# Kernel optimization log

Hardware: AMD Instinct MI355X
Metric: run time of the kernel (lower is better)

## Reference

```python
import jax, jax.numpy as jnp
import numpy as np

REF_MIC = 0
LOAD = 0.001 / np.sqrt(2.0)  # diagonal loading added to both real and imag parts


def _to_complex(x):
    # x: (N, 2, ...) real/imag stacked -> complex (N, ...)
    return x[:, 0] + 1j * x[:, 1]


def setup_inputs() -> dict:
    key = jax.random.key(0)
    k1, k2, k3 = jax.random.split(key, 3)
    N, C, T, F = 8, 16, 300, 257
    mixture = jax.random.normal(k1, (N, 2, C, T, F), dtype=jnp.float32)
    target = jax.random.normal(k2, (N, 2, C, T, F), dtype=jnp.float32)
    steering_vector = jax.random.normal(k3, (N, 2, C, F), dtype=jnp.float32)
    return {"mixture": mixture, "target": target, "steering_vector": steering_vector}


def reference(mixture, target, steering_vector):
    N, _, C, T, F = mixture.shape
    y = _to_complex(mixture)  # (N, C, T, F)
    x = _to_complex(target)   # (N, C, T, F)

    # Spatial covariance of mixture, mean over time frames (sum/T), fused einsum
    # phi[n,f] = (1/T) * sum_t y[n,:,t,f] y[n,:,t,f]^H  -> (N, F, C, C)
    phi = jnp.einsum('nctf,ndtf->nfcd', y, jnp.conj(y)) / T
    eye = jnp.eye(C, dtype=phi.dtype)
    # original adds load to BOTH real and imag diagonals (broadcast over RI dim)
    phi = phi + (LOAD + 1j * LOAD) * eye
    phi_inv = jnp.linalg.inv(phi)  # (N, F, C, C)

    # Cross covariance between mixture and reference-mic target
    A = jnp.transpose(y, (0, 3, 2, 1))            # (N, F, T, C)
    b = jnp.transpose(x[:, REF_MIC], (0, 2, 1))   # (N, F, T)
    mu_a = jnp.mean(A, axis=(0, 2), keepdims=True)  # mean over batch and time
    mu_b = jnp.mean(b, axis=(0, 2), keepdims=True)
    # mean over T of (A-mu_a)(b-mu_b)^H -> (N, F, C)
    phi_yx0 = jnp.mean((A - mu_a) * jnp.conj(b - mu_b)[..., None], axis=2)

    # MWF weights: w = phi_inv @ phi_yx0  -> (N, F, C)
    w = jnp.einsum('nfcd,nfd->nfc', phi_inv, phi_yx0)

    # Beamform: X_bf[n,t,f] = w[n,f]^H y[n,:,t,f]
    Xbf = jnp.einsum('nfc,nctf->ntf', jnp.conj(w), y)  # (N, T, F)

    # Back to real/imag stacked (N, 2, 1, T, F) matching torch output layout
    out = jnp.stack([Xbf.real, Xbf.imag], axis=1)[:, :, None]
    return out
```

## Files before the change

### kernel.cpp

```cpp
#include <hip/hip_runtime.h>

#define N_     8
#define C_     16
#define T_     300
#define F_     257
#define CC_    256
#define TF_    (T_*F_)
#define CTF_   (C_*TF_)
#define N2CTF_ (2*CTF_)

#define FT_    32
#define NFT_   9
#define TS_    5
#define RST_   35
#define SROWS_ 88
#define SCNT_  (SROWS_*RST_)

#define LOADC  7.0710678118654755e-04f

__device__ __forceinline__ float2 cmul(float2 a, float2 b) {
  return make_float2(a.x*b.x - a.y*b.y, a.x*b.y + a.y*b.x);
}
__device__ __forceinline__ float2 cmulc(float2 a, float2 b) {
  return make_float2(a.x*b.x + a.y*b.y, a.y*b.x - a.x*b.y);
}
__device__ __forceinline__ float2 cdiv(float2 a, float2 b) {
  float inv = 1.0f / (b.x*b.x + b.y*b.y);
  return make_float2((a.x*b.x + a.y*b.y)*inv, (a.y*b.x - a.x*b.y)*inv);
}
__device__ __forceinline__ float2 cadd(float2 a, float2 b){ return make_float2(a.x+b.x, a.y+b.y); }
__device__ __forceinline__ float2 csub(float2 a, float2 b){ return make_float2(a.x-b.x, a.y-b.y); }

template<int TCH>
__global__ __launch_bounds__(512, 1) void k1_cov(const float* __restrict__ mix,
                                                 const float* __restrict__ tgt,
                                                 float2* __restrict__ phi_p,
                                                 float2* __restrict__ syx_p,
                                                 float2* __restrict__ sy_p,
                                                 float2* __restrict__ sx_p) {
  __shared__ float2 ys[2][SCNT_];
  const int tid = threadIdx.x;
  const int ft = blockIdx.x, tc = blockIdx.y, n = blockIdx.z;
  const int fbase = ft * FT_;
  const int t0 = tc * TCH;
  const int fl = tid & 31;
  const int g  = tid >> 5;
  const int c0 = (g & 3) * 4;
  const int d0 = (g >> 2) * 4;
  const bool sThread = (g < 4);
  const bool xLoader = (tid < 256);

  const float* mixN = mix + n * N2CTF_;
  const float* tgtN = tgt + n * N2CTF_;

  const int srow = tid >> 5;
  const int f_ld = min(fbase + fl, F_ - 1);
  const float* ybase = mixN + srow * TF_ + f_ld;
  const int xts = min(srow, TS_ - 1);
  const float* xbase = tgtN + f_ld;

  float2 acc[4][4];
  #pragma unroll
  for (int i = 0; i < 4; ++i)
    #pragma unroll
    for (int j = 0; j < 4; ++j) acc[i][j] = make_float2(0.f, 0.f);
  float2 syx[4], sy[4], sx = make_float2(0.f, 0.f);
  #pragma unroll
  for (int i = 0; i < 4; ++i) { syx[i] = make_float2(0.f,0.f); sy[i] = make_float2(0.f,0.f); }

  float lr[6], li[6];
  {
    #pragma unroll
    for (int k = 0; k < TS_; ++k) {
      const float* p = ybase + (t0 + k) * F_;
      lr[k] = p[0]; li[k] = p[CTF_];
    }
    if (xLoader) { const float* p = xbase + (t0 + xts) * F_; lr[5] = p[0]; li[5] = p[CTF_]; }
    #pragma unroll
    for (int k = 0; k < TS_; ++k)
      ys[0][(k * 16 + srow) * RST_ + fl] = make_float2(lr[k], li[k]);
    if (xLoader) ys[0][(80 + srow) * RST_ + fl] = make_float2(lr[5], li[5]);
  }

  constexpr int NS = TCH / TS_;
  for (int stg = 0; stg < NS; ++stg) {
    __syncthreads();
    const bool more = (stg + 1 < NS);
    if (more) {
      const int tS = t0 + (stg + 1) * TS_;
      #pragma unroll
      for (int k = 0; k < TS_; ++k) {
        const float* p = ybase + (tS + k) * F_;
        lr[k] = p[0]; li[k] = p[CTF_];
      }
      if (xLoader) { const float* p = xbase + (tS + xts) * F_; lr[5] = p[0]; li[5] = p[CTF_]; }
    }
    const float2* buf = ys[stg & 1];
    #pragma unroll
    for (int tl = 0; tl < TS_; ++tl) {
      const int rb = tl * 16;
      float2 a[4], b[4];
      #pragma unroll
      for (int i = 0; i < 4; ++i) a[i] = buf[(rb + c0 + i) * RST_ + fl];
      #pragma unroll
      for (int j = 0; j < 4; ++j) b[j] = buf[(rb + d0 + j) * RST_ + fl];
      #pragma unroll
      for (int i = 0; i < 4; ++i)
        #pragma unroll
        for (int j = 0; j < 4; ++j) {
          acc[i][j].x += a[i].x * b[j].x + a[i].y * b[j].y;
          acc[i][j].y += a[i].y * b[j].x - a[i].x * b[j].y;
        }
      if (sThread) {
        float2 xv = buf[(80 + tl) * RST_ + fl];
        #pragma unroll
        for (int i = 0; i < 4; ++i) {
          syx[i].x += a[i].x * xv.x + a[i].y * xv.y;
          syx[i].y += a[i].y * xv.x - a[i].x * xv.y;
          sy[i].x += a[i].x; sy[i].y += a[i].y;
        }
        if (g == 0) { sx.x += xv.x; sx.y += xv.y; }
      }
    }
    if (more) {
      float2* nb = ys[(stg + 1) & 1];
      #pragma unroll
      for (int k = 0; k < TS_; ++k)
        nb[(k * 16 + srow) * RST_ + fl] = make_float2(lr[k], li[k]);
      if (xLoader) nb[(80 + srow) * RST_ + fl] = make_float2(lr[5], li[5]);
    }
  }

  const int f = fbase + fl;
  if (f < F_) {
    const int tcn = tc * N_ + n;
    float2* pb = phi_p + ((size_t)tcn * F_ + f) * CC_;
    #pragma unroll
    for (int i = 0; i < 4; ++i) {
      float2* p = pb + (c0 + i) * 16 + d0;
      #pragma unroll
      for (int j = 0; j < 4; ++j) p[j] = acc[i][j];
    }
    if (sThread) {
      float2* s1 = syx_p + ((size_t)tcn * F_ + f) * C_ + c0;
      float2* s2 = sy_p  + ((size_t)tcn * F_ + f) * C_ + c0;
      #pragma unroll
      for (int i = 0; i < 4; ++i) { s1[i] = syx[i]; s2[i] = sy[i]; }
      if (g == 0) sx_p[(size_t)tcn * F_ + f] = sx;
    }
  }
}

template<int TCP>
__global__ __launch_bounds__(256) void k2_solve(const float2* __restrict__ phi_p,
                                                const float2* __restrict__ syx_p,
                                                const float2* __restrict__ sy_p,
                                                const float2* __restrict__ sx_p,
                                                float* __restrict__ wre,
                                                float* __restrict__ wim) {
  __shared__ float2 M[16 * 17];
  __shared__ float2 fac[16];
  __shared__ float2 ld_sy[TCP * N_ * C_];
  __shared__ float2 ld_syx[TCP * C_];
  __shared__ float2 ld_sx[TCP * N_];
  __shared__ float2 muB_s, sxO_s;
  const int f = blockIdx.x, n = blockIdx.y;
  const int tid = threadIdx.x;
  const int i = tid >> 4, j = tid & 15;

  float2 s = make_float2(0.f, 0.f);
  for (int tc = 0; tc < TCP; ++tc) {
    float2 v = phi_p[((size_t)(tc * N_ + n) * F_ + f) * CC_ + tid];
    s.x += v.x; s.y += v.y;
  }
  if (i == j) { s.x += (float)T_ * LOADC; s.y += (float)T_ * LOADC; }
  M[i * 17 + j] = s;

  for (int idx = tid; idx < TCP * N_ * C_; idx += 256) {
    int tcn = idx >> 4, c = idx & 15;
    ld_sy[idx] = sy_p[((size_t)tcn * F_ + f) * C_ + c];
  }
  for (int idx = tid; idx < TCP * C_; idx += 256) {
    int tc = idx >> 4, c = idx & 15;
    ld_syx[idx] = syx_p[((size_t)(tc * N_ + n) * F_ + f) * C_ + c];
  }
  for (int idx = tid; idx < TCP * N_; idx += 256) {
    ld_sx[idx] = sx_p[(size_t)idx * F_ + f];
  }
  __syncthreads();

  float2 muA_r = make_float2(0.f,0.f), ownY = make_float2(0.f,0.f), ownYX = make_float2(0.f,0.f);
  if (tid < 16) {
    float2 allY = make_float2(0.f,0.f);
    for (int tcn = 0; tcn < TCP * N_; ++tcn) allY = cadd(allY, ld_sy[tcn * C_ + tid]);
    for (int tc = 0; tc < TCP; ++tc) {
      ownY  = cadd(ownY,  ld_sy[(tc * N_ + n) * C_ + tid]);
      ownYX = cadd(ownYX, ld_syx[tc * C_ + tid]);
    }
    const float invNT = 1.0f / ((float)N_ * (float)T_);
    muA_r = make_float2(allY.x * invNT, allY.y * invNT);
  }
  if (tid == 16) {
    float2 own = make_float2(0.f,0.f), all = make_float2(0.f,0.f);
    for (int tc = 0; tc < TCP; ++tc)
      for (int nn = 0; nn < N_; ++nn) {
        float2 v = ld_sx[tc * N_ + nn];
        all = cadd(all, v);
        if (nn == n) own = cadd(own, v);
      }
    const float invNT = 1.0f / ((float)N_ * (float)T_);
    muB_s = make_float2(all.x * invNT, all.y * invNT);
    sxO_s = own;
  }
  __syncthreads();

  if (tid < 16) {
    float2 r = ownYX;
    r = csub(r, cmulc(muA_r, sxO_s));
    r = csub(r, cmulc(ownY, muB_s));
    float2 t3 = cmulc(muA_r, muB_s);
    r.x += (float)T_ * t3.x; r.y += (float)T_ * t3.y;
    M[tid * 17 + 16] = r;
  }
  __syncthreads();

  for (int k = 0; k < 16; ++k) {
    if (tid < 16) {
      fac[tid] = (tid == k) ? make_float2(0.f,0.f)
                            : cdiv(M[tid * 17 + k], M[k * 17 + k]);
    }
    __syncthreads();
    if (i != k) {
      float2 fi = fac[i];
      M[i * 17 + j] = csub(M[i * 17 + j], cmul(fi, M[k * 17 + j]));
      if (j == 15) M[i * 17 + 16] = csub(M[i * 17 + 16], cmul(fi, M[k * 17 + 16]));
    }
    __syncthreads();
  }
  if (tid < 16) {
    float2 w = cdiv(M[tid * 17 + 16], M[tid * 17 + tid]);
    wre[(n * C_ + tid) * F_ + f] = w.x;
    wim[(n * C_ + tid) * F_ + f] = w.y;
  }
}

#define TB3_ 3
__global__ __launch_bounds__(256) void k3_bf(const float* __restrict__ mix,
                                             const float* __restrict__ wre,
                                             const float* __restrict__ wim,
                                             float* __restrict__ out) {
  const int tg = blockIdx.x, n = blockIdx.y;
  const int t0 = tg * TB3_;
  const float* mixN = mix + n * N2CTF_;
  const float* wR = wre + n * C_ * F_;
  const float* wI = wim + n * C_ * F_;
  float* outN = out + n * 2 * TF_;
  for (int f = threadIdx.x; f < F_; f += 256) {
    float wr[16], wi[16];
    #pragma unroll
    for (int c = 0; c < 16; ++c) { wr[c] = wR[c * F_ + f]; wi[c] = wI[c * F_ + f]; }
    #pragma unroll
    for (int tt = 0; tt < TB3_; ++tt) {
      int t = t0 + tt;
      const float* yb = mixN + t * F_ + f;
      float xr = 0.f, xi = 0.f;
      #pragma unroll
      for (int c = 0; c < 16; ++c) {
        float yr = yb[c * TF_];
        float yi = yb[CTF_ + c * TF_];
        xr += wr[c] * yr + wi[c] * yi;
        xi += wr[c] * yi - wi[c] * yr;
      }
      outN[t * F_ + f] = xr;
      outN[TF_ + t * F_ + f] = xi;
    }
  }
}

template<int TCP>
static void launch_all(const float* mix, const float* tgt, float* ws, float* out,
                       hipStream_t stream) {
  constexpr int TCH = T_ / TCP;
  static_assert(TCH * TCP == T_ && TCH % TS_ == 0, "chunking");
  float2* phi_p = (float2*)ws;
  float2* syx_p = phi_p + (size_t)TCP * N_ * F_ * CC_;
  float2* sy_p  = syx_p + (size_t)TCP * N_ * F_ * C_;
  float2* sx_p  = sy_p  + (size_t)TCP * N_ * F_ * C_;
  float*  wre   = (float*)(sx_p + (size_t)TCP * N_ * F_);
  float*  wim   = wre + N_ * C_ * F_;
  k1_cov<TCH><<<dim3(NFT_, TCP, N_), dim3(512), 0, stream>>>(mix, tgt, phi_p, syx_p, sy_p, sx_p);
  k2_solve<TCP><<<dim3(F_, N_), dim3(256), 0, stream>>>(phi_p, syx_p, sy_p, sx_p, wre, wim);
  k3_bf<<<dim3(T_ / TB3_, N_), dim3(256), 0, stream>>>(mix, wre, wim, out);
}

static size_t ws_need_bytes(int tcp) {
  size_t fl = (size_t)tcp * N_ * F_ * (2*CC_ + 2*C_ + 2*C_ + 2) + 2ull * N_ * C_ * F_;
  return fl * 4;
}

extern "C" void kernel_launch(void* const* d_in, const int* in_sizes, int n_in,
                              void* d_out, int out_size, void* d_ws, size_t ws_size,
                              hipStream_t stream) {
  const float* mix = (const float*)d_in[0];
  const float* tgt = (const float*)d_in[1];
  float* out = (float*)d_out;
  float* ws  = (float*)d_ws;
  if (ws_size >= ws_need_bytes(12))      launch_all<12>(mix, tgt, ws, out, stream);
  else if (ws_size >= ws_need_bytes(6))  launch_all<6>(mix, tgt, ws, out, stream);
  else if (ws_size >= ws_need_bytes(2))  launch_all<2>(mix, tgt, ws, out, stream);
  else                                   launch_all<1>(mix, tgt, ws, out, stream);
}
```

Measured before the change: 267.3 us.

## Split solve into reduction and single-wave elimination kernels, simplify beamform

Splits the per-frequency solve into two kernels. The first reduces the partial covariances and cross terms into an augmented matrix stored in global memory. The second runs Gauss-Jordan elimination with a single 64-thread wave, each thread updating four columns, instead of 256 threads with a separate factor array. This is meant to cut idle threads and per-step barrier cost during elimination, at the price of an extra launch and a global round trip for the matrix. The beamform kernel now processes one time frame per block instead of three, giving more blocks but reloading the weights per frame.

```diff
diff --git a/kernel.cpp b/kernel.cpp
--- a/kernel.cpp
+++ b/kernel.cpp
@@ -15,6 +15,8 @@
 #define RST_   35
 #define SROWS_ 88
 #define SCNT_  (SROWS_*RST_)
+
+#define MREC_  272
 
 #define LOADC  7.0710678118654755e-04f
 
@@ -152,14 +154,11 @@
 }
 
 template<int TCP>
-__global__ __launch_bounds__(256) void k2_solve(const float2* __restrict__ phi_p,
-                                                const float2* __restrict__ syx_p,
-                                                const float2* __restrict__ sy_p,
-                                                const float2* __restrict__ sx_p,
-                                                float* __restrict__ wre,
-                                                float* __restrict__ wim) {
-  __shared__ float2 M[16 * 17];
-  __shared__ float2 fac[16];
+__global__ __launch_bounds__(256) void k2a_reduce(const float2* __restrict__ phi_p,
+                                                  const float2* __restrict__ syx_p,
+                                                  const float2* __restrict__ sy_p,
+                                                  const float2* __restrict__ sx_p,
+                                                  float2* __restrict__ Mg) {
   __shared__ float2 ld_sy[TCP * N_ * C_];
   __shared__ float2 ld_syx[TCP * C_];
   __shared__ float2 ld_sx[TCP * N_];
@@ -174,7 +173,6 @@
     s.x += v.x; s.y += v.y;
   }
   if (i == j) { s.x += (float)T_ * LOADC; s.y += (float)T_ * LOADC; }
-  M[i * 17 + j] = s;
 
   for (int idx = tid; idx < TCP * N_ * C_; idx += 256) {
     int tcn = idx >> 4, c = idx & 15;
@@ -214,66 +212,75 @@
   }
   __syncthreads();
 
+  float2* dst = Mg + (size_t)(n * F_ + f) * MREC_;
+  dst[tid] = s;
   if (tid < 16) {
     float2 r = ownYX;
     r = csub(r, cmulc(muA_r, sxO_s));
     r = csub(r, cmulc(ownY, muB_s));
     float2 t3 = cmulc(muA_r, muB_s);
     r.x += (float)T_ * t3.x; r.y += (float)T_ * t3.y;
-    M[tid * 17 + 16] = r;
-  }
+    dst[256 + tid] = r;
+  }
+}
+
+__global__ __launch_bounds__(64) void k2b_solve(const float2* __restrict__ Mg,
+                                                float* __restrict__ wre,
+                                                float* __restrict__ wim) {
+  __shared__ float2 M[16 * 17];
+  const int f = blockIdx.x, n = blockIdx.y;
+  const int tid = threadIdx.x;
+  const float2* src = Mg + (size_t)(n * F_ + f) * MREC_;
+  #pragma unroll
+  for (int r = 0; r < 4; ++r) {
+    int idx = tid + 64 * r;
+    M[(idx >> 4) * 17 + (idx & 15)] = src[idx];
+  }
+  if (tid < 16) M[tid * 17 + 16] = src[256 + tid];
   __syncthreads();
 
+  const int i = tid >> 2, q = tid & 3;
   for (int k = 0; k < 16; ++k) {
-    if (tid < 16) {
-      fac[tid] = (tid == k) ? make_float2(0.f,0.f)
-                            : cdiv(M[tid * 17 + k], M[k * 17 + k]);
-    }
+    float2 fac = cdiv(M[i * 17 + k], M[k * 17 + k]);
     __syncthreads();
     if (i != k) {
-      float2 fi = fac[i];
-      M[i * 17 + j] = csub(M[i * 17 + j], cmul(fi, M[k * 17 + j]));
-      if (j == 15) M[i * 17 + 16] = csub(M[i * 17 + 16], cmul(fi, M[k * 17 + 16]));
+      #pragma unroll
+      for (int jj = 0; jj < 4; ++jj) {
+        int j = q * 4 + jj;
+        M[i * 17 + j] = csub(M[i * 17 + j], cmul(fac, M[k * 17 + j]));
+      }
+      if (q == 3) M[i * 17 + 16] = csub(M[i * 17 + 16], cmul(fac, M[k * 17 + 16]));
     }
     __syncthreads();
   }
-  if (tid < 16) {
-    float2 w = cdiv(M[tid * 17 + 16], M[tid * 17 + tid]);
-    wre[(n * C_ + tid) * F_ + f] = w.x;
-    wim[(n * C_ + tid) * F_ + f] = w.y;
-  }
-}
-
-#define TB3_ 3
+  if (q == 0) {
+    float2 w = cdiv(M[i * 17 + 16], M[i * 17 + i]);
+    wre[(n * C_ + i) * F_ + f] = w.x;
+    wim[(n * C_ + i) * F_ + f] = w.y;
+  }
+}
+
 __global__ __launch_bounds__(256) void k3_bf(const float* __restrict__ mix,
                                              const float* __restrict__ wre,
                                              const float* __restrict__ wim,
                                              float* __restrict__ out) {
-  const int tg = blockIdx.x, n = blockIdx.y;
-  const int t0 = tg * TB3_;
+  const int t = blockIdx.x, n = blockIdx.y;
   const float* mixN = mix + n * N2CTF_;
   const float* wR = wre + n * C_ * F_;
   const float* wI = wim + n * C_ * F_;
   float* outN = out + n * 2 * TF_;
   for (int f = threadIdx.x; f < F_; f += 256) {
-    float wr[16], wi[16];
-    #pragma unroll
-    for (int c = 0; c < 16; ++c) { wr[c] = wR[c * F_ + f]; wi[c] = wI[c * F_ + f]; }
-    #pragma unroll
-    for (int tt = 0; tt < TB3_; ++tt) {
-      int t = t0 + tt;
-      const float* yb = mixN + t * F_ + f;
-      float xr = 0.f, xi = 0.f;
-      #pragma unroll
-      for (int c = 0; c < 16; ++c) {
-        float yr = yb[c * TF_];
-        float yi = yb[CTF_ + c * TF_];
-        xr += wr[c] * yr + wi[c] * yi;
-        xi += wr[c] * yi - wi[c] * yr;
-      }
-      outN[t * F_ + f] = xr;
-      outN[TF_ + t * F_ + f] = xi;
-    }
+    const float* yb = mixN + t * F_ + f;
+    float xr = 0.f, xi = 0.f;
+    #pragma unroll
+    for (int c = 0; c < 16; ++c) {
+      float wr = wR[c * F_ + f], wi = wI[c * F_ + f];
+      float yr = yb[c * TF_],    yi = yb[CTF_ + c * TF_];
+      xr += wr * yr + wi * yi;
+      xi += wr * yi - wi * yr;
+    }
+    outN[t * F_ + f] = xr;
+    outN[TF_ + t * F_ + f] = xi;
   }
 }
 
@@ -286,16 +293,18 @@
   float2* syx_p = phi_p + (size_t)TCP * N_ * F_ * CC_;
   float2* sy_p  = syx_p + (size_t)TCP * N_ * F_ * C_;
   float2* sx_p  = sy_p  + (size_t)TCP * N_ * F_ * C_;
-  float*  wre   = (float*)(sx_p + (size_t)TCP * N_ * F_);
+  float2* Mg    = sx_p  + (size_t)TCP * N_ * F_;
+  float*  wre   = (float*)(Mg + (size_t)N_ * F_ * MREC_);
   float*  wim   = wre + N_ * C_ * F_;
   k1_cov<TCH><<<dim3(NFT_, TCP, N_), dim3(512), 0, stream>>>(mix, tgt, phi_p, syx_p, sy_p, sx_p);
-  k2_solve<TCP><<<dim3(F_, N_), dim3(256), 0, stream>>>(phi_p, syx_p, sy_p, sx_p, wre, wim);
-  k3_bf<<<dim3(T_ / TB3_, N_), dim3(256), 0, stream>>>(mix, wre, wim, out);
+  k2a_reduce<TCP><<<dim3(F_, N_), dim3(256), 0, stream>>>(phi_p, syx_p, sy_p, sx_p, Mg);
+  k2b_solve<<<dim3(F_, N_), dim3(64), 0, stream>>>(Mg, wre, wim);
+  k3_bf<<<dim3(T_, N_), dim3(256), 0, stream>>>(mix, wre, wim, out);
 }
 
 static size_t ws_need_bytes(int tcp) {
-  size_t fl = (size_t)tcp * N_ * F_ * (2*CC_ + 2*C_ + 2*C_ + 2) + 2ull * N_ * C_ * F_;
-  return fl * 4;
+  size_t fl2 = (size_t)tcp * N_ * F_ * (CC_ + C_ + C_ + 1) + (size_t)N_ * F_ * MREC_;
+  return fl2 * 8 + 2ull * N_ * C_ * F_ * 4;
 }
 
 extern "C" void kernel_launch(void* const* d_in, const int* in_sizes, int n_in,
```

Result: faster. 252.0 us (-5.7%).
